# Kernel tuning notes

Hardware: AMD Instinct MI355X
Metric: run time of the kernel (lower is better)

The kernel has to match this reference:

```python
import jax, jax.numpy as jnp
import numpy as np

D_IN = 1024
D_OUT = 1024
NUM_HEADS = 16
HEAD_DIM = D_OUT // NUM_HEADS


def setup_inputs() -> dict:
    key = jax.random.key(0)
    ks = jax.random.split(key, 6)
    B, S = 2, 2048
    x = jax.random.normal(ks[0], (B, S, D_IN), dtype=jnp.float32)
    # nn.Linear stores weight as [out, in]; y = x @ W.T
    scale_in = 1.0 / np.sqrt(D_IN)
    w_query = jax.random.uniform(ks[1], (D_OUT, D_IN), jnp.float32, -scale_in, scale_in)
    w_key = jax.random.uniform(ks[2], (D_OUT, D_IN), jnp.float32, -scale_in, scale_in)
    w_value = jax.random.uniform(ks[3], (D_OUT, D_IN), jnp.float32, -scale_in, scale_in)
    scale_out = 1.0 / np.sqrt(D_OUT)
    w_out = jax.random.uniform(ks[4], (D_OUT, D_OUT), jnp.float32, -scale_out, scale_out)
    b_out = jax.random.uniform(ks[5], (D_OUT,), jnp.float32, -scale_out, scale_out)
    return {"x": x, "w_query": w_query, "w_key": w_key, "w_value": w_value,
            "w_out": w_out, "b_out": b_out}


def reference(x, w_query, w_key, w_value, w_out, b_out):
    B, S, _ = x.shape
    H, Dh = NUM_HEADS, HEAD_DIM
    # projections (no qkv bias), split heads -> [B, H, S, Dh]
    q = (x @ w_query.T).reshape(B, S, H, Dh).transpose(0, 2, 1, 3)
    k = (x @ w_key.T).reshape(B, S, H, Dh).transpose(0, 2, 1, 3)
    v = (x @ w_value.T).reshape(B, S, H, Dh).transpose(0, 2, 1, 3)
    # explicit [B, H, S, S] scores with causal mask (matches masked_fill(triu,-inf))
    scores = jnp.einsum('bhqd,bhkd->bhqk', q, k)
    causal = jnp.tril(jnp.ones((S, S), dtype=bool))  # True = keep
    scores = jnp.where(causal, scores, -jnp.inf)
    attn = jax.nn.softmax(scores / np.sqrt(Dh).astype(np.float32), axis=-1)
    # dropout p=0.0 -> identity
    ctx = jnp.einsum('bhqk,bhkd->bhqd', attn, v)  # [B, H, S, Dh]
    ctx = ctx.transpose(0, 2, 1, 3).reshape(B, S, H * Dh)
    return ctx @ w_out.T + b_out
```

## Files before the change

kernel.cpp:

```cpp
#include <hip/hip_runtime.h>
#include <hip/hip_bf16.h>

typedef __attribute__((ext_vector_type(8))) short short8;
typedef __attribute__((ext_vector_type(4))) short short4_t;
typedef __attribute__((ext_vector_type(8))) float f32x8;
typedef __attribute__((ext_vector_type(4))) float f32x4;

#define MFMA16(a, b, c) __builtin_amdgcn_mfma_f32_16x16x32_bf16((a), (b), (c), 0, 0, 0)


static __device__ __forceinline__ short f2bf(float f) {
    __hip_bfloat16 h = __float2bfloat16(f);
    return *reinterpret_cast<short*>(&h);
}

static __device__ __forceinline__ unsigned pack2bf(float lo, float hi) {
    return ((unsigned)f2bf(lo) & 0xffffu) | ((unsigned)f2bf(hi) << 16);
}

static __device__ __forceinline__ void g2l16(const void* g, void* l) {
    __builtin_amdgcn_global_load_lds(
        (const __attribute__((address_space(1))) void*)g,
        (__attribute__((address_space(3))) void*)l,
        16, 0, 0);
}

__global__ __launch_bounds__(256) void cvt_kernel(
    const float* __restrict__ x,  const float* __restrict__ wq,
    const float* __restrict__ wk, const float* __restrict__ wv,
    const float* __restrict__ wo, __hip_bfloat16* __restrict__ ws)
{
    const size_t e = ((size_t)blockIdx.x * 256 + threadIdx.x) * 8;
    const float* src;
    __hip_bfloat16* dst;
    size_t off;
    if (e < 4194304)      { src = x;  dst = ws + 16777216; off = e; }
    else if (e < 5242880) { src = wq; dst = ws + 20971520; off = e - 4194304; }
    else if (e < 6291456) { src = wk; dst = ws + 20971520 + 1048576; off = e - 5242880; }
    else if (e < 7340032) { src = wv; dst = ws + 20971520 + 2097152; off = e - 6291456; }
    else                  { src = wo; dst = ws + 24117248; off = e - 7340032; }

    f32x8 v = *reinterpret_cast<const f32x8*>(src + off);
    short8 o;
#pragma unroll
    for (int j = 0; j < 8; ++j) o[j] = f2bf(v[j]);
    *reinterpret_cast<short8*>(reinterpret_cast<short*>(dst) + off) = o;
}

__global__ __launch_bounds__(256) void qkv_gemm_kernel(
    const __hip_bfloat16* __restrict__ xbf_,
    const __hip_bfloat16* __restrict__ wqkv_,
    __hip_bfloat16* __restrict__ qkv_out)
{
    const int bid = blockIdx.x;
    const int xcd = bid & 7, kb = bid >> 3;
    const int mBlk = xcd * 4 + (kb / 24);
    const int nBlk = kb % 24;

    const int tid  = threadIdx.x;
    const int lane = tid & 63;
    const int wid  = tid >> 6;
    const int l16  = lane & 15;
    const int lhi  = lane >> 4;
    const int wr = wid >> 1, wc = wid & 1;

    const short* A = reinterpret_cast<const short*>(xbf_);
    const short* Bm = reinterpret_cast<const short*>(wqkv_);
    const int r0A = mBlk * 128, r0B = nBlk * 128;

    __shared__ __align__(16) short sA[128 * 64];
    __shared__ __align__(16) short sB[128 * 64];

    f32x4 acc[4][4] = {};

    for (int kk = 0; kk < 1024; kk += 64) {
#pragma unroll
        for (int it = 0; it < 4; ++it) {
            const int G = it * 256 + tid;
            const int row = G >> 3, gs = G & 7;
            const int gl = gs ^ (row & 7);
            short* lp = sA + (size_t)(it * 256 + wid * 64) * 8;
            g2l16(A + (size_t)(r0A + row) * 1024 + kk + gl * 8, lp);
        }
#pragma unroll
        for (int it = 0; it < 4; ++it) {
            const int G = it * 256 + tid;
            const int row = G >> 3, gs = G & 7;
            const int gl = gs ^ (row & 7);
            short* lp = sB + (size_t)(it * 256 + wid * 64) * 8;
            g2l16(Bm + (size_t)(r0B + row) * 1024 + kk + gl * 8, lp);
        }
        __syncthreads();

#pragma unroll
        for (int ks = 0; ks < 2; ++ks) {
            short8 a[4], b[4];
#pragma unroll
            for (int i = 0; i < 4; ++i) {
                const int row = wr * 64 + i * 16 + l16;
                const int sg = (ks * 4 + lhi) ^ (row & 7);
                a[i] = *reinterpret_cast<const short8*>(&sA[row * 64 + sg * 8]);
            }
#pragma unroll
            for (int j = 0; j < 4; ++j) {
                const int row = wc * 64 + j * 16 + l16;
                const int sg = (ks * 4 + lhi) ^ (row & 7);
                b[j] = *reinterpret_cast<const short8*>(&sB[row * 64 + sg * 8]);
            }
#pragma unroll
            for (int i = 0; i < 4; ++i)
#pragma unroll
                for (int j = 0; j < 4; ++j)
                    acc[i][j] = MFMA16(a[i], b[j], acc[i][j]);
        }
        __syncthreads();
    }

    const int nTileBase = nBlk * 128 + wc * 64;
    const int mat = (nTileBase >> 10);
    __hip_bfloat16* dst = qkv_out + (size_t)mat * 4194304;
    const int mBase = r0A + wr * 64;

    if (mat < 2) {
        const float qscl = (mat == 0) ? 0.18033688f : 1.0f;
#pragma unroll
        for (int i = 0; i < 4; ++i)
#pragma unroll
            for (int j = 0; j < 4; ++j)
#pragma unroll
                for (int r = 0; r < 4; ++r) {
                    const int mRow = mBase + i * 16 + lhi * 4 + r;
                    const int nCol = (nTileBase + j * 16 + l16) & 1023;
                    const int bb = mRow >> 11, s = mRow & 2047;
                    const int h = nCol >> 6, d = nCol & 63;
                    dst[(((size_t)(bb * 16 + h) * 2048 + s) << 6) + d] =
                        __float2bfloat16(acc[i][j][r] * qscl);
                }
    } else {
#pragma unroll
        for (int i = 0; i < 4; ++i) {
            const int mRow0 = mBase + i * 16 + lhi * 4;
            const int bb = mRow0 >> 11, s0 = mRow0 & 2047;
#pragma unroll
            for (int j = 0; j < 4; ++j) {
                const int nCol = (nTileBase + j * 16 + l16) & 1023;
                const int h = nCol >> 6, d = nCol & 63;
                short4_t v4;
#pragma unroll
                for (int r = 0; r < 4; ++r) v4[r] = f2bf(acc[i][j][r]);
                *reinterpret_cast<short4_t*>(
                    reinterpret_cast<short*>(dst) +
                    (((size_t)(bb * 16 + h) * 64 + d) << 11) + s0) = v4;
            }
        }
    }
}

__global__ __launch_bounds__(512, 4) void attn_kernel(
    const __hip_bfloat16* __restrict__ qkv,
    __hip_bfloat16* __restrict__ ctx)
{
    const int tid  = threadIdx.x;
    const int lane = tid & 63;
    const int wid  = tid >> 6;
    const int l16 = lane & 15;
    const int lhi = lane >> 4;

    const int bid = blockIdx.x;
    const int xcd = bid & 7, idx = bid >> 3;
    const int h4 = idx & 3, tg = idx >> 2;
    const int bh = xcd * 4 + h4;
    const int g  = 15 - tg;
    const int qt = g * 8 + wid;
    const int q0 = qt * 16;
    const int sd = q0 >> 6;
    const int ns_blk = 2 * g + 2;

    const short* Q  = reinterpret_cast<const short*>(qkv) + (size_t)bh * 131072;
    const short* K  = Q + 4194304;
    const short* Vt = Q + 8388608;

    __shared__ __align__(16) short sK[2][64 * 64];
    __shared__ __align__(16) short sV[2][64 * 64];
    __shared__ __align__(16) short p_lds_all[8][16 * 72];
    short* p_lds = p_lds_all[wid];

    const int bb = bh >> 4, h = bh & 15;

    short8 qf[2];
    qf[0] = *reinterpret_cast<const short8*>(Q + (size_t)(q0 + l16) * 64 + lhi * 8);
    qf[1] = *reinterpret_cast<const short8*>(Q + (size_t)(q0 + l16) * 64 + 32 + lhi * 8);

    f32x4 oacc[4] = {};
    float lsum = 0.0f;

    const int srow = tid >> 3, sgs = tid & 7;
    const int sgl = sgs ^ (srow & 7);
    auto stage = [&](int buf, int kv0) {
        g2l16(K + (size_t)(kv0 + srow) * 64 + sgl * 8, &sK[buf][(size_t)tid * 8]);
        g2l16(Vt + (size_t)srow * 2048 + kv0 + sgl * 8, &sV[buf][(size_t)tid * 8]);
    };

    stage(0, 0);
    asm volatile("s_waitcnt vmcnt(0)" ::: "memory");
    __syncthreads();

    const int r7 = l16 & 7;
    int cur = 0;
#pragma unroll 1
    for (int st = 0; st < ns_blk; ++st) {
        const int kv0 = st * 64;
        if (st + 1 < ns_blk) stage(cur ^ 1, kv0 + 64);

        if (st <= sd) {
            f32x4 sc[4];
#pragma unroll
            for (int nt = 0; nt < 4; ++nt) {
                f32x4 s = {};
#pragma unroll
                for (int ks = 0; ks < 2; ++ks) {
                    const int sg = (ks * 4 + lhi) ^ r7;
                    short8 kb = *reinterpret_cast<const short8*>(
                        &sK[cur][(nt * 16 + l16) * 64 + sg * 8]);
                    s = MFMA16(kb, qf[ks], s);
                }
                sc[nt] = s;
            }

            if (st == sd) {
#pragma unroll
                for (int nt = 0; nt < 4; ++nt) {
                    const int kvb = kv0 + nt * 16 + lhi * 4;
                    const int qrow = q0 + l16;
#pragma unroll
                    for (int r = 0; r < 4; ++r)
                        if (kvb + r > qrow) sc[nt][r] = -1.0e38f;
                }
            }
#pragma unroll
            for (int nt = 0; nt < 4; ++nt) {
                const float p0 = exp2f(sc[nt][0]);
                const float p1 = exp2f(sc[nt][1]);
                const float p2 = exp2f(sc[nt][2]);
                const float p3 = exp2f(sc[nt][3]);
                lsum += (p0 + p1) + (p2 + p3);
                uint2 w;
                w.x = pack2bf(p0, p1);
                w.y = pack2bf(p2, p3);
                *reinterpret_cast<uint2*>(&p_lds[l16 * 72 + nt * 16 + lhi * 4]) = w;
            }
            asm volatile("s_waitcnt lgkmcnt(0)" ::: "memory");

#pragma unroll
            for (int ks = 0; ks < 2; ++ks) {
                short8 pf = *reinterpret_cast<const short8*>(
                    &p_lds[l16 * 72 + ks * 32 + lhi * 8]);
#pragma unroll
                for (int dt = 0; dt < 4; ++dt) {
                    const int sg = (ks * 4 + lhi) ^ r7;
                    short8 vb = *reinterpret_cast<const short8*>(
                        &sV[cur][(dt * 16 + l16) * 64 + sg * 8]);
                    oacc[dt] = MFMA16(pf, vb, oacc[dt]);
                }
            }
        }

        asm volatile("s_waitcnt vmcnt(0)" ::: "memory");
        __syncthreads();
        cur ^= 1;
    }

    float rs = lsum;
    rs += __shfl_xor(rs, 16);
    rs += __shfl_xor(rs, 32);
    const float rinvq = 1.0f / rs;
    float rinv[4];
#pragma unroll
    for (int r = 0; r < 4; ++r) rinv[r] = __shfl(rinvq, lhi * 4 + r);

#pragma unroll
    for (int dt = 0; dt < 4; ++dt)
#pragma unroll
        for (int r = 0; r < 4; ++r) {
            const int q = q0 + lhi * 4 + r;
            ctx[((size_t)bb * 2048 + q) * 1024 + h * 64 + dt * 16 + l16] =
                __float2bfloat16(oacc[dt][r] * rinv[r]);
        }
}

__global__ __launch_bounds__(256) void out_gemm_kernel(
    const __hip_bfloat16* __restrict__ ctx,
    const __hip_bfloat16* __restrict__ wobf,
    const float* __restrict__ bo,
    float* __restrict__ out)
{
    const int bid = blockIdx.x;
    const int xcd = bid & 7, kb = bid >> 3;
    const int mBlk = xcd * 4 + (kb >> 3);
    const int nBlk = kb & 7;

    const int tid  = threadIdx.x;
    const int lane = tid & 63;
    const int wid  = tid >> 6;
    const int l16  = lane & 15;
    const int lhi  = lane >> 4;
    const int wr = wid >> 1, wc = wid & 1;

    const short* A = reinterpret_cast<const short*>(ctx);
    const short* Bm = reinterpret_cast<const short*>(wobf);
    const int r0A = mBlk * 128, r0B = nBlk * 128;

    __shared__ __align__(16) short sA[128 * 64];
    __shared__ __align__(16) short sB[128 * 64];

    f32x4 acc[4][4] = {};

    for (int kk = 0; kk < 1024; kk += 64) {
#pragma unroll
        for (int it = 0; it < 4; ++it) {
            const int G = it * 256 + tid;
            const int row = G >> 3, gs = G & 7;
            const int gl = gs ^ (row & 7);
            short* lp = sA + (size_t)(it * 256 + wid * 64) * 8;
            g2l16(A + (size_t)(r0A + row) * 1024 + kk + gl * 8, lp);
        }
#pragma unroll
        for (int it = 0; it < 4; ++it) {
            const int G = it * 256 + tid;
            const int row = G >> 3, gs = G & 7;
            const int gl = gs ^ (row & 7);
            short* lp = sB + (size_t)(it * 256 + wid * 64) * 8;
            g2l16(Bm + (size_t)(r0B + row) * 1024 + kk + gl * 8, lp);
        }
        __syncthreads();

#pragma unroll
        for (int ks = 0; ks < 2; ++ks) {
            short8 a[4], b[4];
#pragma unroll
            for (int i = 0; i < 4; ++i) {
                const int row = wr * 64 + i * 16 + l16;
                const int sg = (ks * 4 + lhi) ^ (row & 7);
                a[i] = *reinterpret_cast<const short8*>(&sA[row * 64 + sg * 8]);
            }
#pragma unroll
            for (int j = 0; j < 4; ++j) {
                const int row = wc * 64 + j * 16 + l16;
                const int sg = (ks * 4 + lhi) ^ (row & 7);
                b[j] = *reinterpret_cast<const short8*>(&sB[row * 64 + sg * 8]);
            }
#pragma unroll
            for (int i = 0; i < 4; ++i)
#pragma unroll
                for (int j = 0; j < 4; ++j)
                    acc[i][j] = MFMA16(a[i], b[j], acc[i][j]);
        }
        __syncthreads();
    }

    const int mBase = r0A + wr * 64;
    const int nBase = r0B + wc * 64;
#pragma unroll
    for (int i = 0; i < 4; ++i)
#pragma unroll
        for (int j = 0; j < 4; ++j)
#pragma unroll
            for (int r = 0; r < 4; ++r) {
                const int mRow = mBase + i * 16 + lhi * 4 + r;
                const int nCol = nBase + j * 16 + l16;
                out[(size_t)mRow * 1024 + nCol] = acc[i][j][r] + bo[nCol];
            }
}

extern "C" void kernel_launch(void* const* d_in, const int* in_sizes, int n_in,
                              void* d_out, int out_size, void* d_ws, size_t ws_size,
                              hipStream_t stream) {
    const float* x  = (const float*)d_in[0];
    const float* wq = (const float*)d_in[1];
    const float* wk = (const float*)d_in[2];
    const float* wv = (const float*)d_in[3];
    const float* wo = (const float*)d_in[4];
    const float* bo = (const float*)d_in[5];

    __hip_bfloat16* ws = (__hip_bfloat16*)d_ws;
    __hip_bfloat16* ctx  = ws + 12582912;
    __hip_bfloat16* xbf  = ws + 16777216;
    __hip_bfloat16* wqkv = ws + 20971520;
    __hip_bfloat16* wobf = ws + 24117248;
    float* out = (float*)d_out;

    cvt_kernel<<<4096, 256, 0, stream>>>(x, wq, wk, wv, wo, ws);
    qkv_gemm_kernel<<<768, 256, 0, stream>>>(xbf, wqkv, ws);
    attn_kernel<<<512, 512, 0, stream>>>(ws, ctx);
    out_gemm_kernel<<<256, 256, 0, stream>>>(ctx, wobf, bo, out);
}
```

Measured before the change: 119.7 us.

## Double-buffer LDS in QKV and output GEMMs, swap MFMA operands for vectorized Q/K stores

Both GEMM kernels now use two LDS buffers of half the K-depth (32 instead of 64), so the global-to-LDS prefetch of the next K slice is issued before the MFMAs on the current one. This hides load latency behind compute. In the QKV kernel, Q and K tiles swap the MFMA operands so each lane holds four consecutive head-dim values, letting the epilogue write 8-byte vector stores instead of scalar bf16 stores. The smaller K step doubles the number of barriers and waitcnt points per kernel.

```diff
diff --git a/kernel.cpp b/kernel.cpp
--- a/kernel.cpp
+++ b/kernel.cpp
@@ -68,74 +68,90 @@
     const short* Bm = reinterpret_cast<const short*>(wqkv_);
     const int r0A = mBlk * 128, r0B = nBlk * 128;
 
-    __shared__ __align__(16) short sA[128 * 64];
-    __shared__ __align__(16) short sB[128 * 64];
+    const int nTileBase = nBlk * 128 + wc * 64;
+    const int mat = (nTileBase >> 10);
+    const bool swp = (mat < 2);
+
+    __shared__ __align__(16) short sA[2][128 * 32];
+    __shared__ __align__(16) short sB[2][128 * 32];
 
     f32x4 acc[4][4] = {};
 
-    for (int kk = 0; kk < 1024; kk += 64) {
-#pragma unroll
-        for (int it = 0; it < 4; ++it) {
+    auto stage = [&](int buf, int kk) {
+#pragma unroll
+        for (int it = 0; it < 2; ++it) {
             const int G = it * 256 + tid;
-            const int row = G >> 3, gs = G & 7;
-            const int gl = gs ^ (row & 7);
-            short* lp = sA + (size_t)(it * 256 + wid * 64) * 8;
-            g2l16(A + (size_t)(r0A + row) * 1024 + kk + gl * 8, lp);
-        }
-#pragma unroll
-        for (int it = 0; it < 4; ++it) {
-            const int G = it * 256 + tid;
-            const int row = G >> 3, gs = G & 7;
-            const int gl = gs ^ (row & 7);
-            short* lp = sB + (size_t)(it * 256 + wid * 64) * 8;
-            g2l16(Bm + (size_t)(r0B + row) * 1024 + kk + gl * 8, lp);
-        }
-        __syncthreads();
-
-#pragma unroll
-        for (int ks = 0; ks < 2; ++ks) {
-            short8 a[4], b[4];
-#pragma unroll
-            for (int i = 0; i < 4; ++i) {
-                const int row = wr * 64 + i * 16 + l16;
-                const int sg = (ks * 4 + lhi) ^ (row & 7);
-                a[i] = *reinterpret_cast<const short8*>(&sA[row * 64 + sg * 8]);
-            }
-#pragma unroll
-            for (int j = 0; j < 4; ++j) {
-                const int row = wc * 64 + j * 16 + l16;
-                const int sg = (ks * 4 + lhi) ^ (row & 7);
-                b[j] = *reinterpret_cast<const short8*>(&sB[row * 64 + sg * 8]);
-            }
+            const int row = G >> 2, gs = G & 3;
+            const int gl = gs ^ (row & 3);
+            g2l16(A + (size_t)(r0A + row) * 1024 + kk + gl * 8,
+                  &sA[buf][(size_t)G * 8]);
+            g2l16(Bm + (size_t)(r0B + row) * 1024 + kk + gl * 8,
+                  &sB[buf][(size_t)G * 8]);
+        }
+    };
+
+    stage(0, 0);
+    asm volatile("s_waitcnt vmcnt(0)" ::: "memory");
+    __syncthreads();
+
+    int cur = 0;
+#pragma unroll 1
+    for (int kk = 0; kk < 1024; kk += 32) {
+        if (kk + 32 < 1024) stage(cur ^ 1, kk + 32);
+
+        short8 a[4], b[4];
+#pragma unroll
+        for (int i = 0; i < 4; ++i) {
+            const int row = wr * 64 + i * 16 + l16;
+            const int sg = lhi ^ (row & 3);
+            a[i] = *reinterpret_cast<const short8*>(&sA[cur][row * 32 + sg * 8]);
+        }
+#pragma unroll
+        for (int j = 0; j < 4; ++j) {
+            const int row = wc * 64 + j * 16 + l16;
+            const int sg = lhi ^ (row & 3);
+            b[j] = *reinterpret_cast<const short8*>(&sB[cur][row * 32 + sg * 8]);
+        }
+        if (swp) {
+#pragma unroll
+            for (int i = 0; i < 4; ++i)
+#pragma unroll
+                for (int j = 0; j < 4; ++j)
+                    acc[i][j] = MFMA16(b[j], a[i], acc[i][j]);
+        } else {
 #pragma unroll
             for (int i = 0; i < 4; ++i)
 #pragma unroll
                 for (int j = 0; j < 4; ++j)
                     acc[i][j] = MFMA16(a[i], b[j], acc[i][j]);
         }
+
+        asm volatile("s_waitcnt vmcnt(0)" ::: "memory");
         __syncthreads();
+        cur ^= 1;
     }
 
-    const int nTileBase = nBlk * 128 + wc * 64;
-    const int mat = (nTileBase >> 10);
     __hip_bfloat16* dst = qkv_out + (size_t)mat * 4194304;
     const int mBase = r0A + wr * 64;
 
-    if (mat < 2) {
+    if (swp) {
         const float qscl = (mat == 0) ? 0.18033688f : 1.0f;
 #pragma unroll
-        for (int i = 0; i < 4; ++i)
-#pragma unroll
-            for (int j = 0; j < 4; ++j)
-#pragma unroll
-                for (int r = 0; r < 4; ++r) {
-                    const int mRow = mBase + i * 16 + lhi * 4 + r;
-                    const int nCol = (nTileBase + j * 16 + l16) & 1023;
-                    const int bb = mRow >> 11, s = mRow & 2047;
-                    const int h = nCol >> 6, d = nCol & 63;
-                    dst[(((size_t)(bb * 16 + h) * 2048 + s) << 6) + d] =
-                        __float2bfloat16(acc[i][j][r] * qscl);
-                }
+        for (int i = 0; i < 4; ++i) {
+            const int mRow = mBase + i * 16 + l16;
+            const int bb = mRow >> 11, s = mRow & 2047;
+#pragma unroll
+            for (int j = 0; j < 4; ++j) {
+                const int nCol0 = (nTileBase + j * 16 + lhi * 4) & 1023;
+                const int h = nCol0 >> 6, d0 = nCol0 & 63;
+                short4_t v4;
+#pragma unroll
+                for (int r = 0; r < 4; ++r) v4[r] = f2bf(acc[i][j][r] * qscl);
+                *reinterpret_cast<short4_t*>(
+                    reinterpret_cast<short*>(dst) +
+                    (((size_t)(bb * 16 + h) * 2048 + s) << 6) + d0) = v4;
+            }
+        }
     } else {
 #pragma unroll
         for (int i = 0; i < 4; ++i) {
@@ -310,52 +326,55 @@
     const short* Bm = reinterpret_cast<const short*>(wobf);
     const int r0A = mBlk * 128, r0B = nBlk * 128;
 
-    __shared__ __align__(16) short sA[128 * 64];
-    __shared__ __align__(16) short sB[128 * 64];
+    __shared__ __align__(16) short sA[2][128 * 32];
+    __shared__ __align__(16) short sB[2][128 * 32];
 
     f32x4 acc[4][4] = {};
 
-    for (int kk = 0; kk < 1024; kk += 64) {
-#pragma unroll
-        for (int it = 0; it < 4; ++it) {
+    auto stage = [&](int buf, int kk) {
+#pragma unroll
+        for (int it = 0; it < 2; ++it) {
             const int G = it * 256 + tid;
-            const int row = G >> 3, gs = G & 7;
-            const int gl = gs ^ (row & 7);
-            short* lp = sA + (size_t)(it * 256 + wid * 64) * 8;
-            g2l16(A + (size_t)(r0A + row) * 1024 + kk + gl * 8, lp);
-        }
-#pragma unroll
-        for (int it = 0; it < 4; ++it) {
-            const int G = it * 256 + tid;
-            const int row = G >> 3, gs = G & 7;
-            const int gl = gs ^ (row & 7);
-            short* lp = sB + (size_t)(it * 256 + wid * 64) * 8;
-            g2l16(Bm + (size_t)(r0B + row) * 1024 + kk + gl * 8, lp);
-        }
+            const int row = G >> 2, gs = G & 3;
+            const int gl = gs ^ (row & 3);
+            g2l16(A + (size_t)(r0A + row) * 1024 + kk + gl * 8,
+                  &sA[buf][(size_t)G * 8]);
+            g2l16(Bm + (size_t)(r0B + row) * 1024 + kk + gl * 8,
+                  &sB[buf][(size_t)G * 8]);
+        }
+    };
+
+    stage(0, 0);
+    asm volatile("s_waitcnt vmcnt(0)" ::: "memory");
+    __syncthreads();
+
+    int cur = 0;
+#pragma unroll 1
+    for (int kk = 0; kk < 1024; kk += 32) {
+        if (kk + 32 < 1024) stage(cur ^ 1, kk + 32);
+
+        short8 a[4], b[4];
+#pragma unroll
+        for (int i = 0; i < 4; ++i) {
+            const int row = wr * 64 + i * 16 + l16;
+            const int sg = lhi ^ (row & 3);
+            a[i] = *reinterpret_cast<const short8*>(&sA[cur][row * 32 + sg * 8]);
+        }
+#pragma unroll
+        for (int j = 0; j < 4; ++j) {
+            const int row = wc * 64 + j * 16 + l16;
+            const int sg = lhi ^ (row & 3);
+            b[j] = *reinterpret_cast<const short8*>(&sB[cur][row * 32 + sg * 8]);
+        }
+#pragma unroll
+        for (int i = 0; i < 4; ++i)
+#pragma unroll
+            for (int j = 0; j < 4; ++j)
+                acc[i][j] = MFMA16(a[i], b[j], acc[i][j]);
+
+        asm volatile("s_waitcnt vmcnt(0)" ::: "memory");
         __syncthreads();
-
-#pragma unroll
-        for (int ks = 0; ks < 2; ++ks) {
-            short8 a[4], b[4];
-#pragma unroll
-            for (int i = 0; i < 4; ++i) {
-                const int row = wr * 64 + i * 16 + l16;
-                const int sg = (ks * 4 + lhi) ^ (row & 7);
-                a[i] = *reinterpret_cast<const short8*>(&sA[row * 64 + sg * 8]);
-            }
-#pragma unroll
-            for (int j = 0; j < 4; ++j) {
-                const int row = wc * 64 + j * 16 + l16;
-                const int sg = (ks * 4 + lhi) ^ (row & 7);
-                b[j] = *reinterpret_cast<const short8*>(&sB[row * 64 + sg * 8]);
-            }
-#pragma unroll
-            for (int i = 0; i < 4; ++i)
-#pragma unroll
-                for (int j = 0; j < 4; ++j)
-                    acc[i][j] = MFMA16(a[i], b[j], acc[i][j]);
-        }
-        __syncthreads();
+        cur ^= 1;
     }
 
     const int mBase = r0A + wr * 64;
```

New measurement: 135.2 us. 1.13x slower.
